# Kernel optimization log

Measured on AMD Instinct MI355X. Metric: run time of the kernel, lower is better.

The kernel has to match this reference:

```python
import math
import jax, jax.numpy as jnp
import numpy as np

S, H, E = 8192, 4096, 64          # tokens, hidden, experts
CAPACITY_FACTOR = 1.0
MIN_CAPACITY = 4


def setup_inputs() -> dict:
    key = jax.random.key(0)
    k1, k2 = jax.random.split(key)
    return {
        "gate_input": jax.random.normal(k1, (S, H), dtype=jnp.float32),
        "gate_weight": jax.random.normal(k2, (E, H), dtype=jnp.float32) * 0.02,
    }


def reference(gate_input, gate_weight):
    # Router projection (always fp32, bias-free Linear)
    logits = gate_input.astype(jnp.float32) @ gate_weight.astype(jnp.float32).T  # [S, E]
    gates = jax.nn.softmax(logits, axis=1)
    s, e = gates.shape
    # _capacity with capacity_factor*2 for top-2; static given shapes
    capacity = max(int(math.ceil(s * (CAPACITY_FACTOR * 2.0) / e)), MIN_CAPACITY)

    # top-2 expert selection
    _, sel = jax.lax.top_k(gates, 2)                       # [S, 2]
    mask1 = jax.nn.one_hot(sel[:, 0], e, dtype=jnp.int32)  # [S, E]
    mask2 = jax.nn.one_hot(sel[:, 1], e, dtype=jnp.int32)

    # cumsum-based slot assignment within each expert
    loc1 = jnp.cumsum(mask1, axis=0) - 1
    loc2 = jnp.cumsum(mask2, axis=0) - 1 + jnp.sum(mask1, axis=0, keepdims=True)

    # aux load-balancing loss (aux_loss_coef = 0 -> no gate rescale)
    me = jnp.mean(gates, axis=0)
    ce = jnp.mean(mask1.astype(jnp.float32), axis=0)
    l_aux = jnp.mean(me * ce) * e * e

    # drop tokens over capacity
    mask1 = mask1 * (loc1 < capacity).astype(jnp.int32)
    mask2 = mask2 * (loc2 < capacity).astype(jnp.int32)
    idx_in_exp1 = jnp.sum(loc1 * mask1, axis=1)            # [S]
    idx_in_exp2 = jnp.sum(loc2 * mask2, axis=1)

    m1f = mask1.astype(jnp.float32)
    m2f = mask2.astype(jnp.float32)
    w1 = jnp.max(gates * m1f, axis=1)
    w2 = jnp.max(gates * m2f, axis=1)
    denom = jnp.maximum(w1 + w2, jnp.finfo(jnp.float32).eps)
    w1 = w1 / denom
    w2 = w2 / denom

    gates1 = w1[:, None] * m1f                             # [S, E]
    gates2 = w2[:, None] * m2f
    loc1_sc = jax.nn.one_hot(idx_in_exp1, capacity, dtype=jnp.float32)  # [S, C]
    loc2_sc = jax.nn.one_hot(idx_in_exp2, capacity, dtype=jnp.float32)
    combine_weights = (gates1[:, :, None] * loc1_sc[:, None, :]
                       + gates2[:, :, None] * loc2_sc[:, None, :])      # [S, E, C]
    dispatch_mask = combine_weights > 0
    return l_aux, combine_weights, dispatch_mask
```

## Files before the change

kernel.cpp:

```cpp
#include <hip/hip_runtime.h>
#include <cstdint>
#include <cstddef>

constexpr int S = 8192;
constexpr int H = 4096;
constexpr int E = 64;
constexpr int CAP = 256;
constexpr int KSPLIT = 4;
constexpr int KCHUNK = H / KSPLIT;
constexpr int BK = 32;
constexpr int BM = 64;
constexpr long long SEC = (long long)S * E * CAP;

__global__ __launch_bounds__(256)
void k_gemm(const float* __restrict__ A, const float* __restrict__ W,
            float* __restrict__ part) {
    __shared__ float As[BK][BM + 4];
    __shared__ float Bs[BK][E + 4];
    const int tid = threadIdx.x;
    const int m0 = blockIdx.x * BM;
    const int kbase = blockIdx.y * KCHUNK;
    const int lr = tid >> 3;
    const int lc = (tid & 7) << 2;
    const int ty = tid >> 4;
    const int tx = tid & 15;

    float acc[4][4];
#pragma unroll
    for (int i = 0; i < 4; ++i)
#pragma unroll
        for (int j = 0; j < 4; ++j) acc[i][j] = 0.f;

    for (int kc = 0; kc < KCHUNK; kc += BK) {
        const float* ap = A + (size_t)(m0 + lr) * H + (kbase + kc + lc);
        const float4 av0 = *(const float4*)ap;
        const float4 av1 = *(const float4*)(ap + (size_t)32 * H);
        const float* bp = W + (size_t)lr * H + (kbase + kc + lc);
        const float4 bv0 = *(const float4*)bp;
        const float4 bv1 = *(const float4*)(bp + (size_t)32 * H);
        __syncthreads();
        As[lc + 0][lr] = av0.x; As[lc + 1][lr] = av0.y;
        As[lc + 2][lr] = av0.z; As[lc + 3][lr] = av0.w;
        As[lc + 0][lr + 32] = av1.x; As[lc + 1][lr + 32] = av1.y;
        As[lc + 2][lr + 32] = av1.z; As[lc + 3][lr + 32] = av1.w;
        Bs[lc + 0][lr] = bv0.x; Bs[lc + 1][lr] = bv0.y;
        Bs[lc + 2][lr] = bv0.z; Bs[lc + 3][lr] = bv0.w;
        Bs[lc + 0][lr + 32] = bv1.x; Bs[lc + 1][lr + 32] = bv1.y;
        Bs[lc + 2][lr + 32] = bv1.z; Bs[lc + 3][lr + 32] = bv1.w;
        __syncthreads();
#pragma unroll
        for (int kk = 0; kk < BK; ++kk) {
            const float4 a = *(const float4*)&As[kk][ty * 4];
            const float4 b = *(const float4*)&Bs[kk][tx * 4];
            acc[0][0] = fmaf(a.x, b.x, acc[0][0]);
            acc[0][1] = fmaf(a.x, b.y, acc[0][1]);
            acc[0][2] = fmaf(a.x, b.z, acc[0][2]);
            acc[0][3] = fmaf(a.x, b.w, acc[0][3]);
            acc[1][0] = fmaf(a.y, b.x, acc[1][0]);
            acc[1][1] = fmaf(a.y, b.y, acc[1][1]);
            acc[1][2] = fmaf(a.y, b.z, acc[1][2]);
            acc[1][3] = fmaf(a.y, b.w, acc[1][3]);
            acc[2][0] = fmaf(a.z, b.x, acc[2][0]);
            acc[2][1] = fmaf(a.z, b.y, acc[2][1]);
            acc[2][2] = fmaf(a.z, b.z, acc[2][2]);
            acc[2][3] = fmaf(a.z, b.w, acc[2][3]);
            acc[3][0] = fmaf(a.w, b.x, acc[3][0]);
            acc[3][1] = fmaf(a.w, b.y, acc[3][1]);
            acc[3][2] = fmaf(a.w, b.z, acc[3][2]);
            acc[3][3] = fmaf(a.w, b.w, acc[3][3]);
        }
    }
    float* P = part + (size_t)blockIdx.y * S * E;
#pragma unroll
    for (int i = 0; i < 4; ++i) {
        float4 v = make_float4(acc[i][0], acc[i][1], acc[i][2], acc[i][3]);
        *(float4*)&P[(size_t)(m0 + ty * 4 + i) * E + tx * 4] = v;
    }
}

__global__ __launch_bounds__(256)
void k_router(const float* __restrict__ part, int* __restrict__ e1a,
              int* __restrict__ e2a, float* __restrict__ g1a,
              float* __restrict__ g2a, float* __restrict__ sumg,
              int* __restrict__ cnt1) {
    const int lane = threadIdx.x & 63;
    const int gw = blockIdx.x * 4 + (threadIdx.x >> 6);
    float lsum = 0.f;
    int lcnt = 0;
    for (int s = gw; s < S; s += 256) {
        const float* p = part + (size_t)s * E + lane;
        float l = p[0] + p[(size_t)S * E] + p[2 * (size_t)S * E]
                + p[3 * (size_t)S * E];
        float m = l;
#pragma unroll
        for (int o = 32; o; o >>= 1) m = fmaxf(m, __shfl_xor(m, o));
        const float ex = __expf(l - m);
        float Z = ex;
#pragma unroll
        for (int o = 32; o; o >>= 1) Z += __shfl_xor(Z, o);
        const float g = ex / Z;
        lsum += g;
        float v1 = g; int i1 = lane;
#pragma unroll
        for (int o = 32; o; o >>= 1) {
            const float ov = __shfl_xor(v1, o);
            const int oi = __shfl_xor(i1, o);
            if (ov > v1 || (ov == v1 && oi < i1)) { v1 = ov; i1 = oi; }
        }
        float v2 = (lane == i1) ? -1.f : g; int i2 = lane;
#pragma unroll
        for (int o = 32; o; o >>= 1) {
            const float ov = __shfl_xor(v2, o);
            const int oi = __shfl_xor(i2, o);
            if (ov > v2 || (ov == v2 && oi < i2)) { v2 = ov; i2 = oi; }
        }
        if (i1 == lane) lcnt++;
        if (lane == 0) {
            e1a[s] = i1; e2a[s] = i2; g1a[s] = v1; g2a[s] = v2;
        }
    }
    atomicAdd(&sumg[lane], lsum);
    atomicAdd(&cnt1[lane], lcnt);
}

__global__ __launch_bounds__(64)
void k_assign(const int* __restrict__ e1a, const int* __restrict__ e2a,
              int* __restrict__ slot1a, int* __restrict__ slot2a) {
    const int e = blockIdx.x;
    const int lane = threadIdx.x;
    const unsigned long long below = (1ull << lane) - 1ull;
    int cnt = 0;
    for (int c = 0; c < S; c += 64) {
        const int s = c + lane;
        const bool m = (e1a[s] == e);
        const unsigned long long bal = __ballot(m);
        if (m) {
            const int rank = cnt + __popcll(bal & below);
            slot1a[s] = (rank < CAP) ? rank : -1;
        }
        cnt += __popcll(bal);
    }
    const int total1 = cnt;
    int cnt2 = 0;
    for (int c = 0; c < S; c += 64) {
        const int s = c + lane;
        const bool m = (e2a[s] == e);
        const unsigned long long bal = __ballot(m);
        if (m) {
            const int rank = total1 + cnt2 + __popcll(bal & below);
            slot2a[s] = (rank < CAP) ? rank : -1;
        }
        cnt2 += __popcll(bal);
    }
}

__global__ __launch_bounds__(256)
void k_scatter(const int* __restrict__ e1a, const int* __restrict__ e2a,
               const float* __restrict__ g1a, const float* __restrict__ g2a,
               const int* __restrict__ slot1a, const int* __restrict__ slot2a,
               float* __restrict__ out) {
    const int s = blockIdx.x * 256 + threadIdx.x;
    float* comb = out + 1;
    float* mask = out + 1 + (size_t)SEC;
    const int sl1 = slot1a[s], sl2 = slot2a[s];
    const float w1 = (sl1 >= 0) ? g1a[s] : 0.f;
    const float w2 = (sl2 >= 0) ? g2a[s] : 0.f;
    const float denom = fmaxf(w1 + w2, 1.1920928955078125e-07f);
    if (sl1 >= 0) {
        const float w = w1 / denom;
        const size_t off = ((size_t)s * E + e1a[s]) * CAP + sl1;
        comb[off] = w;
        if (w > 0.f) mask[off] = 1.f;
    }
    if (sl2 >= 0) {
        const float w = w2 / denom;
        const size_t off = ((size_t)s * E + e2a[s]) * CAP + sl2;
        comb[off] = w;
        if (w > 0.f) mask[off] = 1.f;
    }
}

__global__ __launch_bounds__(64)
void k_aux(const float* __restrict__ sumg, const int* __restrict__ cnt1,
           float* __restrict__ out) {
    const int lane = threadIdx.x;
    float v = sumg[lane] * (float)cnt1[lane];
#pragma unroll
    for (int o = 32; o; o >>= 1) v += __shfl_xor(v, o);
    if (lane == 0) out[0] = v * (float)E / ((float)S * (float)S);
}

extern "C" void kernel_launch(void* const* d_in, const int* in_sizes, int n_in,
                              void* d_out, int out_size, void* d_ws,
                              size_t ws_size, hipStream_t stream) {
    const float* A = (const float*)d_in[0];
    const float* W = (const float*)d_in[1];
    float* out = (float*)d_out;

    char* ws = (char*)d_ws;
    float* part = (float*)ws;
    size_t off = (size_t)KSPLIT * S * E * sizeof(float);
    int* e1a = (int*)(ws + off);      off += (size_t)S * 4;
    int* e2a = (int*)(ws + off);      off += (size_t)S * 4;
    float* g1a = (float*)(ws + off);  off += (size_t)S * 4;
    float* g2a = (float*)(ws + off);  off += (size_t)S * 4;
    int* slot1a = (int*)(ws + off);   off += (size_t)S * 4;
    int* slot2a = (int*)(ws + off);   off += (size_t)S * 4;
    float* sumg = (float*)(ws + off); off += (size_t)E * 4;
    int* cnt1 = (int*)(ws + off);     off += (size_t)E * 4;

    hipMemsetAsync(sumg, 0, 2 * (size_t)E * 4, stream);
    hipMemsetAsync(d_out, 0, (size_t)out_size * sizeof(float), stream);

    k_gemm<<<dim3(S / BM, KSPLIT), 256, 0, stream>>>(A, W, part);
    k_router<<<64, 256, 0, stream>>>(part, e1a, e2a, g1a, g2a, sumg, cnt1);
    k_assign<<<E, 64, 0, stream>>>(e1a, e2a, slot1a, slot2a);
    k_scatter<<<S / 256, 256, 0, stream>>>(e1a, e2a, g1a, g2a, slot1a, slot2a,
                                           out);
    k_aux<<<1, 64, 0, stream>>>(sumg, cnt1, out);
}
```

Before: 1.276 ms.

## Fuse output zero-fill with dense combine/mask write, drop full-output memset

Replaces the whole-output memset followed by a sparse scatter kernel with one kernel that writes every combine-weight and dispatch-mask element for each token, placing the nonzero values inline. This removes the separate memset pass and the scattered writes that came after it. The output is written once by compute threads instead of by the memset engine, and each thread issues scalar stores, which may be less efficient than a memset.

```diff
diff --git a/kernel.cpp b/kernel.cpp
--- a/kernel.cpp
+++ b/kernel.cpp
@@ -10,6 +10,7 @@
 constexpr int KCHUNK = H / KSPLIT;
 constexpr int BK = 32;
 constexpr int BM = 64;
+constexpr int EC = E * CAP;
 constexpr long long SEC = (long long)S * E * CAP;
 
 __global__ __launch_bounds__(256)
@@ -155,28 +156,41 @@
 }
 
 __global__ __launch_bounds__(256)
-void k_scatter(const int* __restrict__ e1a, const int* __restrict__ e2a,
-               const float* __restrict__ g1a, const float* __restrict__ g2a,
-               const int* __restrict__ slot1a, const int* __restrict__ slot2a,
-               float* __restrict__ out) {
-    const int s = blockIdx.x * 256 + threadIdx.x;
-    float* comb = out + 1;
-    float* mask = out + 1 + (size_t)SEC;
+void k_write(const int* __restrict__ e1a, const int* __restrict__ e2a,
+             const float* __restrict__ g1a, const float* __restrict__ g2a,
+             const int* __restrict__ slot1a, const int* __restrict__ slot2a,
+             float* __restrict__ out) {
+    const int s = blockIdx.x;
+    const int t = threadIdx.x;
     const int sl1 = slot1a[s], sl2 = slot2a[s];
     const float w1 = (sl1 >= 0) ? g1a[s] : 0.f;
     const float w2 = (sl2 >= 0) ? g2a[s] : 0.f;
     const float denom = fmaxf(w1 + w2, 1.1920928955078125e-07f);
-    if (sl1 >= 0) {
-        const float w = w1 / denom;
-        const size_t off = ((size_t)s * E + e1a[s]) * CAP + sl1;
-        comb[off] = w;
-        if (w > 0.f) mask[off] = 1.f;
-    }
-    if (sl2 >= 0) {
-        const float w = w2 / denom;
-        const size_t off = ((size_t)s * E + e2a[s]) * CAP + sl2;
-        comb[off] = w;
-        if (w > 0.f) mask[off] = 1.f;
+    const float w1n = w1 / denom;
+    const float w2n = w2 / denom;
+    const int off1 = (sl1 >= 0) ? e1a[s] * CAP + sl1 : -1;
+    const int off2 = (sl2 >= 0) ? e2a[s] * CAP + sl2 : -1;
+    float* __restrict__ comb = out + 1 + (size_t)s * EC;
+    float* __restrict__ mask = comb + (size_t)SEC;
+#pragma unroll
+    for (int it = 0; it < EC / 1024; ++it) {
+        const int lo = it << 10;
+        const int base = lo + (t << 2);
+        const bool hit = ((unsigned)(off1 - lo) < 1024u) |
+                         ((unsigned)(off2 - lo) < 1024u);
+        float v0 = 0.f, v1 = 0.f, v2 = 0.f, v3 = 0.f;
+        if (hit) {
+            v0 = (base + 0 == off1) ? w1n : (base + 0 == off2) ? w2n : 0.f;
+            v1 = (base + 1 == off1) ? w1n : (base + 1 == off2) ? w2n : 0.f;
+            v2 = (base + 2 == off1) ? w1n : (base + 2 == off2) ? w2n : 0.f;
+            v3 = (base + 3 == off1) ? w1n : (base + 3 == off2) ? w2n : 0.f;
+        }
+        comb[base + 0] = v0; comb[base + 1] = v1;
+        comb[base + 2] = v2; comb[base + 3] = v3;
+        mask[base + 0] = (v0 > 0.f) ? 1.f : 0.f;
+        mask[base + 1] = (v1 > 0.f) ? 1.f : 0.f;
+        mask[base + 2] = (v2 > 0.f) ? 1.f : 0.f;
+        mask[base + 3] = (v3 > 0.f) ? 1.f : 0.f;
     }
 }
 
@@ -210,12 +224,10 @@
     int* cnt1 = (int*)(ws + off);     off += (size_t)E * 4;
 
     hipMemsetAsync(sumg, 0, 2 * (size_t)E * 4, stream);
-    hipMemsetAsync(d_out, 0, (size_t)out_size * sizeof(float), stream);
 
     k_gemm<<<dim3(S / BM, KSPLIT), 256, 0, stream>>>(A, W, part);
     k_router<<<64, 256, 0, stream>>>(part, e1a, e2a, g1a, g2a, sumg, cnt1);
     k_assign<<<E, 64, 0, stream>>>(e1a, e2a, slot1a, slot2a);
-    k_scatter<<<S / 256, 256, 0, stream>>>(e1a, e2a, g1a, g2a, slot1a, slot2a,
-                                           out);
+    k_write<<<S, 256, 0, stream>>>(e1a, e2a, g1a, g2a, slot1a, slot2a, out);
     k_aux<<<1, 64, 0, stream>>>(sumg, cnt1, out);
 }
```

After: 1.309 ms. 2.6% more time.

## Fuse output zero-fill into router GEMM and fold aux loss into scatter

Applied to the files above, without the earlier changes.

The separate hipMemsetAsync of the roughly 1 GB combine/dispatch output is removed. Each GEMM block now writes its share of zeros with nontemporal float4 stores, interleaved with its K-loop iterations, so the bandwidth-bound fill overlaps the FMA-bound projection. The aux-loss reduction kernel is folded into the scatter kernel to save a launch, and the redundant w>0 check before writing the mask is dropped. The risk is that the zero stores contend with the GEMM's global loads, and that write ordering now depends on GEMM blocks finishing before scatter runs.

```diff
diff --git a/kernel.cpp b/kernel.cpp
--- a/kernel.cpp
+++ b/kernel.cpp
@@ -11,27 +11,37 @@
 constexpr int BK = 32;
 constexpr int BM = 64;
 constexpr long long SEC = (long long)S * E * CAP;
+constexpr long long OUTN = 2 * SEC + 1;
+constexpr int F4_PER_BLOCK = 131072;
+constexpr int F4_PER_ITER = 16;
+
+typedef float f4_t __attribute__((ext_vector_type(4)));
 
 __global__ __launch_bounds__(256)
-void k_gemm(const float* __restrict__ A, const float* __restrict__ W,
-            float* __restrict__ part) {
+void k_gemm_fill(const float* __restrict__ A, const float* __restrict__ W,
+                 float* __restrict__ part, float* __restrict__ out) {
     __shared__ float As[BK][BM + 4];
     __shared__ float Bs[BK][E + 4];
     const int tid = threadIdx.x;
     const int m0 = blockIdx.x * BM;
     const int kbase = blockIdx.y * KCHUNK;
+    const int b = blockIdx.y * gridDim.x + blockIdx.x;
     const int lr = tid >> 3;
     const int lc = (tid & 7) << 2;
     const int ty = tid >> 4;
     const int tx = tid & 15;
 
+    f4_t* __restrict__ fill = (f4_t*)out + (size_t)b * F4_PER_BLOCK + tid;
+    const f4_t z4 = {0.f, 0.f, 0.f, 0.f};
+
     float acc[4][4];
 #pragma unroll
     for (int i = 0; i < 4; ++i)
 #pragma unroll
         for (int j = 0; j < 4; ++j) acc[i][j] = 0.f;
 
-    for (int kc = 0; kc < KCHUNK; kc += BK) {
+    for (int it = 0; it < KCHUNK / BK; ++it) {
+        const int kc = it * BK;
         const float* ap = A + (size_t)(m0 + lr) * H + (kbase + kc + lc);
         const float4 av0 = *(const float4*)ap;
         const float4 av1 = *(const float4*)(ap + (size_t)32 * H);
@@ -48,28 +58,33 @@
         Bs[lc + 0][lr + 32] = bv1.x; Bs[lc + 1][lr + 32] = bv1.y;
         Bs[lc + 2][lr + 32] = bv1.z; Bs[lc + 3][lr + 32] = bv1.w;
         __syncthreads();
+        f4_t* d = fill + (size_t)it * (F4_PER_ITER * 256);
+#pragma unroll
+        for (int j = 0; j < F4_PER_ITER; ++j)
+            __builtin_nontemporal_store(z4, d + j * 256);
 #pragma unroll
         for (int kk = 0; kk < BK; ++kk) {
             const float4 a = *(const float4*)&As[kk][ty * 4];
-            const float4 b = *(const float4*)&Bs[kk][tx * 4];
-            acc[0][0] = fmaf(a.x, b.x, acc[0][0]);
-            acc[0][1] = fmaf(a.x, b.y, acc[0][1]);
-            acc[0][2] = fmaf(a.x, b.z, acc[0][2]);
-            acc[0][3] = fmaf(a.x, b.w, acc[0][3]);
-            acc[1][0] = fmaf(a.y, b.x, acc[1][0]);
-            acc[1][1] = fmaf(a.y, b.y, acc[1][1]);
-            acc[1][2] = fmaf(a.y, b.z, acc[1][2]);
-            acc[1][3] = fmaf(a.y, b.w, acc[1][3]);
-            acc[2][0] = fmaf(a.z, b.x, acc[2][0]);
-            acc[2][1] = fmaf(a.z, b.y, acc[2][1]);
-            acc[2][2] = fmaf(a.z, b.z, acc[2][2]);
-            acc[2][3] = fmaf(a.z, b.w, acc[2][3]);
-            acc[3][0] = fmaf(a.w, b.x, acc[3][0]);
-            acc[3][1] = fmaf(a.w, b.y, acc[3][1]);
-            acc[3][2] = fmaf(a.w, b.z, acc[3][2]);
-            acc[3][3] = fmaf(a.w, b.w, acc[3][3]);
-        }
-    }
+            const float4 bb = *(const float4*)&Bs[kk][tx * 4];
+            acc[0][0] = fmaf(a.x, bb.x, acc[0][0]);
+            acc[0][1] = fmaf(a.x, bb.y, acc[0][1]);
+            acc[0][2] = fmaf(a.x, bb.z, acc[0][2]);
+            acc[0][3] = fmaf(a.x, bb.w, acc[0][3]);
+            acc[1][0] = fmaf(a.y, bb.x, acc[1][0]);
+            acc[1][1] = fmaf(a.y, bb.y, acc[1][1]);
+            acc[1][2] = fmaf(a.y, bb.z, acc[1][2]);
+            acc[1][3] = fmaf(a.y, bb.w, acc[1][3]);
+            acc[2][0] = fmaf(a.z, bb.x, acc[2][0]);
+            acc[2][1] = fmaf(a.z, bb.y, acc[2][1]);
+            acc[2][2] = fmaf(a.z, bb.z, acc[2][2]);
+            acc[2][3] = fmaf(a.z, bb.w, acc[2][3]);
+            acc[3][0] = fmaf(a.w, bb.x, acc[3][0]);
+            acc[3][1] = fmaf(a.w, bb.y, acc[3][1]);
+            acc[3][2] = fmaf(a.w, bb.z, acc[3][2]);
+            acc[3][3] = fmaf(a.w, bb.w, acc[3][3]);
+        }
+    }
+    if (b == 0 && tid == 0) out[(size_t)OUTN - 1] = 0.f;
     float* P = part + (size_t)blockIdx.y * S * E;
 #pragma unroll
     for (int i = 0; i < 4; ++i) {
@@ -158,6 +173,7 @@
 void k_scatter(const int* __restrict__ e1a, const int* __restrict__ e2a,
                const float* __restrict__ g1a, const float* __restrict__ g2a,
                const int* __restrict__ slot1a, const int* __restrict__ slot2a,
+               const float* __restrict__ sumg, const int* __restrict__ cnt1,
                float* __restrict__ out) {
     const int s = blockIdx.x * 256 + threadIdx.x;
     float* comb = out + 1;
@@ -167,27 +183,22 @@
     const float w2 = (sl2 >= 0) ? g2a[s] : 0.f;
     const float denom = fmaxf(w1 + w2, 1.1920928955078125e-07f);
     if (sl1 >= 0) {
-        const float w = w1 / denom;
         const size_t off = ((size_t)s * E + e1a[s]) * CAP + sl1;
-        comb[off] = w;
-        if (w > 0.f) mask[off] = 1.f;
+        comb[off] = w1 / denom;
+        mask[off] = 1.f;
     }
     if (sl2 >= 0) {
-        const float w = w2 / denom;
         const size_t off = ((size_t)s * E + e2a[s]) * CAP + sl2;
-        comb[off] = w;
-        if (w > 0.f) mask[off] = 1.f;
-    }
-}
-
-__global__ __launch_bounds__(64)
-void k_aux(const float* __restrict__ sumg, const int* __restrict__ cnt1,
-           float* __restrict__ out) {
-    const int lane = threadIdx.x;
-    float v = sumg[lane] * (float)cnt1[lane];
-#pragma unroll
-    for (int o = 32; o; o >>= 1) v += __shfl_xor(v, o);
-    if (lane == 0) out[0] = v * (float)E / ((float)S * (float)S);
+        comb[off] = w2 / denom;
+        mask[off] = 1.f;
+    }
+    if (blockIdx.x == 0 && threadIdx.x < 64) {
+        const int lane = threadIdx.x;
+        float v = sumg[lane] * (float)cnt1[lane];
+#pragma unroll
+        for (int o = 32; o; o >>= 1) v += __shfl_xor(v, o);
+        if (lane == 0) out[0] = v * (float)E / ((float)S * (float)S);
+    }
 }
 
 extern "C" void kernel_launch(void* const* d_in, const int* in_sizes, int n_in,
@@ -210,12 +221,10 @@
     int* cnt1 = (int*)(ws + off);     off += (size_t)E * 4;
 
     hipMemsetAsync(sumg, 0, 2 * (size_t)E * 4, stream);
-    hipMemsetAsync(d_out, 0, (size_t)out_size * sizeof(float), stream);
-
-    k_gemm<<<dim3(S / BM, KSPLIT), 256, 0, stream>>>(A, W, part);
+
+    k_gemm_fill<<<dim3(S / BM, KSPLIT), 256, 0, stream>>>(A, W, part, out);
     k_router<<<64, 256, 0, stream>>>(part, e1a, e2a, g1a, g2a, sumg, cnt1);
     k_assign<<<E, 64, 0, stream>>>(e1a, e2a, slot1a, slot2a);
     k_scatter<<<S / 256, 256, 0, stream>>>(e1a, e2a, g1a, g2a, slot1a, slot2a,
-                                           out);
-    k_aux<<<1, 64, 0, stream>>>(sumg, cnt1, out);
-}
+                                           sumg, cnt1, out);
+}
```

Result: slower. 1.319 ms (+3.4%).
